# Kernel optimization log

Measured on AMD Instinct MI355X. Metric: run time of the kernel, lower is better.

Reference implementation:

```python
import jax, jax.numpy as jnp
import numpy as np

EMBED_DIM = 1024
NUM_HEADS = 16
HEAD_DIM = EMBED_DIM // NUM_HEADS
WINDOW = 128


def setup_inputs() -> dict:
    key = jax.random.key(0)
    ks = jax.random.split(key, 9)
    B, T, C = 1, 2048, EMBED_DIM
    s = 1.0 / np.sqrt(C)
    inp = {
        "x": jax.random.normal(ks[0], (B, T, C), dtype=jnp.float32),
        "wq": jax.random.normal(ks[1], (C, C), dtype=jnp.float32) * s,
        "bq": jnp.zeros((C,), dtype=jnp.float32),
        "wk": jax.random.normal(ks[2], (C, C), dtype=jnp.float32) * s,
        "bk": jnp.zeros((C,), dtype=jnp.float32),
        "wv": jax.random.normal(ks[3], (C, C), dtype=jnp.float32) * s,
        "bv": jnp.zeros((C,), dtype=jnp.float32),
        "wo": jax.random.normal(ks[4], (C, C), dtype=jnp.float32) * s,
        "bo": jnp.zeros((C,), dtype=jnp.float32),
    }
    return inp


def reference(x, wq, bq, wk, bk, wv, bv, wo, bo):
    B, T, C = x.shape
    H, D, W = NUM_HEADS, HEAD_DIM, WINDOW

    def proj(w, b):
        # torch Linear: y = x @ w.T + b ; -> (B, H, T, D)
        return (x @ w.T + b).reshape(B, T, H, D).transpose(0, 2, 1, 3)

    q = proj(wq, bq)
    k = proj(wk, bk)
    v = proj(wv, bv)

    # window index map: position t attends to keys [t-W+1, t]; zero-padded before 0
    idx = jnp.arange(T)[:, None] + jnp.arange(W)[None, :] - (W - 1)  # (T, W)
    valid = (idx >= 0)
    idxc = jnp.clip(idx, 0, T - 1)

    kw = k[:, :, idxc]                                 # (B, H, T, W, D)
    vw = v[:, :, idxc] * valid[None, None, :, :, None]  # zero padded values

    # zero-key padding gives raw score exactly 0 (inside the softmax)
    scores = jnp.einsum('bhtd,bhtwd->bhtw', q, kw)
    scores = jnp.where(valid[None, None], scores, 0.0) / np.sqrt(D)
    attn = jax.nn.softmax(scores, axis=-1)             # (B, H, T, W)

    ctx = jnp.einsum('bhtw,bhtwd->bhtd', attn, vw)     # (B, H, T, D)
    out = ctx.transpose(0, 2, 1, 3).reshape(B, T, C)
    return out @ wo.T + bo
```

## Files before the change

### kernel.cpp

```cpp
#include <hip/hip_runtime.h>


#define TSEQ 2048
#define CDIM 1024
#define HNUM 16
#define DHEAD 64
#define WWIN 128

typedef __attribute__((ext_vector_type(8))) short bf16x8;
typedef __attribute__((ext_vector_type(4))) float f32x4;

__device__ __forceinline__ unsigned short f2bf(float f) {
  unsigned u = __float_as_uint(f);
  u = (u + 0x7fffu + ((u >> 16) & 1u)) >> 16;
  return (unsigned short)u;
}
__device__ __forceinline__ float bf2f(unsigned short s) {
  return __uint_as_float(((unsigned)s) << 16);
}

__device__ __forceinline__ void gload16(const void* g, void* l) {
  __builtin_amdgcn_global_load_lds(
      (const __attribute__((address_space(1))) unsigned int*)g,
      (__attribute__((address_space(3))) unsigned int*)l, 16, 0, 0);
}

__global__ void split_bf16(const float* s0, const float* s1, const float* s2,
                           const float* s3,
                           unsigned short* h0, unsigned short* h1,
                           unsigned short* h2, unsigned short* h3,
                           unsigned short* l0, unsigned short* l1,
                           unsigned short* l2, unsigned short* l3, int n4) {
  const int z = blockIdx.z;
  const float* __restrict__ src = z == 0 ? s0 : (z == 1 ? s1 : (z == 2 ? s2 : s3));
  unsigned short* __restrict__ h = z == 0 ? h0 : (z == 1 ? h1 : (z == 2 ? h2 : h3));
  unsigned short* __restrict__ l = z == 0 ? l0 : (z == 1 ? l1 : (z == 2 ? l2 : l3));
  const int i = blockIdx.x * 256 + threadIdx.x;
  if (i >= n4) return;
  const float4 v = ((const float4*)src)[i];
  ushort4 hh, ll;
  hh.x = f2bf(v.x); ll.x = f2bf(v.x - bf2f(hh.x));
  hh.y = f2bf(v.y); ll.y = f2bf(v.y - bf2f(hh.y));
  hh.z = f2bf(v.z); ll.z = f2bf(v.z - bf2f(hh.z));
  hh.w = f2bf(v.w); ll.w = f2bf(v.w - bf2f(hh.w));
  ((ushort4*)h)[i] = hh;
  ((ushort4*)l)[i] = ll;
}

__launch_bounds__(256, 2)
__global__ void gemm_mfma_split(const unsigned short* __restrict__ Ah,
                                const unsigned short* __restrict__ Al,
                                const unsigned short* Bh0, const unsigned short* Bh1,
                                const unsigned short* Bh2,
                                const unsigned short* Bl0, const unsigned short* Bl1,
                                const unsigned short* Bl2,
                                const float* bias0, const float* bias1, const float* bias2,
                                float* C0, float* C1, float* C2,
                                int M, int N, int K) {
  const int z = blockIdx.z;
  const unsigned short* __restrict__ Bh = z == 0 ? Bh0 : (z == 1 ? Bh1 : Bh2);
  const unsigned short* __restrict__ Bl = z == 0 ? Bl0 : (z == 1 ? Bl1 : Bl2);
  const float* __restrict__ bias = z == 0 ? bias0 : (z == 1 ? bias1 : bias2);
  float* __restrict__ C = z == 0 ? C0 : (z == 1 ? C1 : C2);

  __shared__ unsigned short lAh[128 * 32], lAl[128 * 32];
  __shared__ unsigned short lBh[128 * 32], lBl[128 * 32];

  const int tid = threadIdx.x;
  const int w = tid >> 6, lane = tid & 63;
  const int wr = w >> 1, wc = w & 1;
  const int bm = blockIdx.y * 128, bn = blockIdx.x * 128;

  int srow[2], scol[2], soff[2];
#pragma unroll
  for (int q = 0; q < 2; ++q) {
    const int s = w * 128 + q * 64 + lane;
    const int r = s >> 2;
    srow[q] = r;
    scol[q] = ((s & 3) ^ ((r >> 1) & 3)) * 8;
    soff[q] = (w * 128 + q * 64) * 8;
  }
  int aoff[4], boff[4];
#pragma unroll
  for (int i = 0; i < 4; ++i) {
    const int ra = wr * 64 + i * 16 + (lane & 15);
    aoff[i] = ra * 32 + (((lane >> 4) ^ ((ra >> 1) & 3)) * 8);
    const int rb = wc * 64 + i * 16 + (lane & 15);
    boff[i] = rb * 32 + (((lane >> 4) ^ ((rb >> 1) & 3)) * 8);
  }

  f32x4 acc[4][4];
#pragma unroll
  for (int i = 0; i < 4; ++i)
#pragma unroll
    for (int j = 0; j < 4; ++j) acc[i][j] = {0.f, 0.f, 0.f, 0.f};

  const unsigned short* gAh = Ah + (size_t)bm * K;
  const unsigned short* gAl = Al + (size_t)bm * K;
  const unsigned short* gBh = Bh + (size_t)bn * K;
  const unsigned short* gBl = Bl + (size_t)bn * K;

  for (int k0 = 0; k0 < K; k0 += 32) {
#pragma unroll
    for (int q = 0; q < 2; ++q) {
      const size_t go = (size_t)srow[q] * K + k0 + scol[q];
      gload16(gAh + go, &lAh[soff[q]]);
      gload16(gAl + go, &lAl[soff[q]]);
      gload16(gBh + go, &lBh[soff[q]]);
      gload16(gBl + go, &lBl[soff[q]]);
    }
    __syncthreads();

    bf16x8 fah[4], fal[4], fbh[4], fbl[4];
#pragma unroll
    for (int i = 0; i < 4; ++i) {
      fah[i] = *(const bf16x8*)&lAh[aoff[i]];
      fal[i] = *(const bf16x8*)&lAl[aoff[i]];
      fbh[i] = *(const bf16x8*)&lBh[boff[i]];
      fbl[i] = *(const bf16x8*)&lBl[boff[i]];
    }
#pragma unroll
    for (int i = 0; i < 4; ++i)
#pragma unroll
      for (int j = 0; j < 4; ++j) {
        acc[i][j] = __builtin_amdgcn_mfma_f32_16x16x32_bf16(fah[i], fbh[j], acc[i][j], 0, 0, 0);
        acc[i][j] = __builtin_amdgcn_mfma_f32_16x16x32_bf16(fah[i], fbl[j], acc[i][j], 0, 0, 0);
        acc[i][j] = __builtin_amdgcn_mfma_f32_16x16x32_bf16(fal[i], fbh[j], acc[i][j], 0, 0, 0);
      }
    __syncthreads();
  }

  const int colb = bn + wc * 64 + (lane & 15);
  const int rowb = bm + wr * 64 + ((lane >> 4) << 2);
#pragma unroll
  for (int j = 0; j < 4; ++j) {
    const int col = colb + j * 16;
    const float bv = bias[col];
#pragma unroll
    for (int i = 0; i < 4; ++i) {
      const int row = rowb + i * 16;
#pragma unroll
      for (int r = 0; r < 4; ++r)
        C[(size_t)(row + r) * N + col] = acc[i][j][r] + bv;
    }
  }
}

__launch_bounds__(256, 2)
__global__ void gemm_bt(const float* __restrict__ A,
                        const float* __restrict__ Bw0, const float* __restrict__ Bw1,
                        const float* __restrict__ Bw2,
                        const float* __restrict__ bias0, const float* __restrict__ bias1,
                        const float* __restrict__ bias2,
                        float* __restrict__ C0, float* __restrict__ C1, float* __restrict__ C2,
                        int M, int N, int K) {
  const int z = blockIdx.z;
  const float* __restrict__ B = (z == 0) ? Bw0 : ((z == 1) ? Bw1 : Bw2);
  const float* __restrict__ bias = (z == 0) ? bias0 : ((z == 1) ? bias1 : bias2);
  float* __restrict__ C = (z == 0) ? C0 : ((z == 1) ? C1 : C2);

  __shared__ float As[16][132];
  __shared__ float Bs[16][132];

  const int tid = threadIdx.x;
  const int tx = tid & 15;
  const int ty = tid >> 4;
  const int bm = blockIdx.y * 128;
  const int bn = blockIdx.x * 128;
  const int lrow = tid >> 2;
  const int lk = (tid & 3) << 2;

  float acc[8][8] = {};

  for (int k0 = 0; k0 < K; k0 += 16) {
#pragma unroll
    for (int r = 0; r < 2; ++r) {
      const int row = (r << 6) + lrow;
      const float4 a4 = *(const float4*)(A + (size_t)(bm + row) * K + k0 + lk);
      As[lk + 0][row] = a4.x; As[lk + 1][row] = a4.y;
      As[lk + 2][row] = a4.z; As[lk + 3][row] = a4.w;
      const float4 b4 = *(const float4*)(B + (size_t)(bn + row) * K + k0 + lk);
      Bs[lk + 0][row] = b4.x; Bs[lk + 1][row] = b4.y;
      Bs[lk + 2][row] = b4.z; Bs[lk + 3][row] = b4.w;
    }
    __syncthreads();
#pragma unroll
    for (int k = 0; k < 16; ++k) {
      float a[8], b[8];
      *(float4*)(a)     = *(const float4*)(&As[k][ty * 8]);
      *(float4*)(a + 4) = *(const float4*)(&As[k][ty * 8 + 4]);
      *(float4*)(b)     = *(const float4*)(&Bs[k][tx * 8]);
      *(float4*)(b + 4) = *(const float4*)(&Bs[k][tx * 8 + 4]);
#pragma unroll
      for (int i = 0; i < 8; ++i)
#pragma unroll
        for (int j = 0; j < 8; ++j)
          acc[i][j] = fmaf(a[i], b[j], acc[i][j]);
    }
    __syncthreads();
  }

#pragma unroll
  for (int i = 0; i < 8; ++i) {
    const int row = bm + ty * 8 + i;
#pragma unroll
    for (int j4 = 0; j4 < 2; ++j4) {
      const int col = bn + tx * 8 + j4 * 4;
      const float4 bb = *(const float4*)(bias + col);
      float4 o;
      o.x = acc[i][j4 * 4 + 0] + bb.x;
      o.y = acc[i][j4 * 4 + 1] + bb.y;
      o.z = acc[i][j4 * 4 + 2] + bb.z;
      o.w = acc[i][j4 * 4 + 3] + bb.w;
      *(float4*)(C + (size_t)row * N + col) = o;
    }
  }
}

__launch_bounds__(256)
__global__ void swa_attn(const float* __restrict__ Q, const float* __restrict__ K,
                         const float* __restrict__ V, float* __restrict__ Of,
                         unsigned short* __restrict__ Oh, unsigned short* __restrict__ Ol,
                         int pack) {
  __shared__ float kb[144 * 64];
  __shared__ float qs[16 * 64];
  __shared__ float ps[4 * 4 * 132];

  const int h = blockIdx.y;
  const int t0 = blockIdx.x * 16;
  const int tid = threadIdx.x;
  const int hoff = h * DHEAD;

  for (int i = tid; i < 144 * 16; i += 256) {
    const int x = i >> 4;
    const int cp = i & 15;
    const int c = cp ^ (x & 15);
    const int key = t0 - (WWIN - 1) + x;
    float4 kv = make_float4(0.f, 0.f, 0.f, 0.f);
    if (key >= 0 && key < TSEQ)
      kv = *(const float4*)(K + (size_t)key * CDIM + hoff + 4 * c);
    *(float4*)&kb[x * 64 + 4 * cp] = kv;
  }
  for (int i = tid; i < 16 * 16; i += 256) {
    const int xq = i >> 4;
    const int c = i & 15;
    *(float4*)&qs[xq * 64 + 4 * c] =
        *(const float4*)(Q + (size_t)(t0 + xq) * CDIM + hoff + 4 * c);
  }
  for (int i = tid; i < 4 * 4 * 132; i += 256) ps[i] = 0.f;
  __syncthreads();

  const int w = tid >> 6;
  const int lane = tid & 63;
  const int q0 = w * 4;

  float inv[4];

#pragma unroll
  for (int q = 0; q < 4; ++q) {
    const int xl = q0 + q + lane;
    const int xm = xl & 15;
    const float* kp0 = kb + xl * 64;
    const float* kp1 = kp0 + 64 * 64;
    const float* qp = qs + (q0 + q) * 64;
    float s0 = 0.f, s1 = 0.f;
#pragma unroll
    for (int dc = 0; dc < 16; ++dc) {
      const float4 qv = *(const float4*)(qp + 4 * dc);
      const int co = 4 * (dc ^ xm);
      const float4 k0 = *(const float4*)(kp0 + co);
      const float4 k1 = *(const float4*)(kp1 + co);
      s0 = fmaf(qv.x, k0.x, fmaf(qv.y, k0.y, fmaf(qv.z, k0.z, fmaf(qv.w, k0.w, s0))));
      s1 = fmaf(qv.x, k1.x, fmaf(qv.y, k1.y, fmaf(qv.z, k1.z, fmaf(qv.w, k1.w, s1))));
    }
    s0 *= 0.125f;
    s1 *= 0.125f;

    float m = fmaxf(s0, s1);
#pragma unroll
    for (int off = 32; off > 0; off >>= 1) m = fmaxf(m, __shfl_xor(m, off));
    const float p0 = __expf(s0 - m);
    const float p1 = __expf(s1 - m);
    float sum = p0 + p1;
#pragma unroll
    for (int off = 32; off > 0; off >>= 1) sum += __shfl_xor(sum, off);
    inv[q] = 1.0f / sum;

    float* psq = ps + (w * 4 + q) * 132;
    psq[q + lane] = p0;
    psq[q + 64 + lane] = p1;
  }

  float accq[4] = {0.f, 0.f, 0.f, 0.f};
  const float* psb = ps + w * 4 * 132;
#pragma unroll 4
  for (int ci = 0; ci < 33; ++ci) {
    const int xr = 4 * ci;
    const float4 pq0 = *(const float4*)(psb + 0 * 132 + xr);
    const float4 pq1 = *(const float4*)(psb + 1 * 132 + xr);
    const float4 pq2 = *(const float4*)(psb + 2 * 132 + xr);
    const float4 pq3 = *(const float4*)(psb + 3 * 132 + xr);
#pragma unroll
    for (int xi = 0; xi < 4; ++xi) {
      const int x = q0 + xr + xi;
      const int key = t0 - (WWIN - 1) + x;
      float vx = 0.f;
      if (key >= 0) {
        const int kc = key < TSEQ ? key : TSEQ - 1;
        vx = V[(size_t)kc * CDIM + hoff + lane];
      }
      const float f0 = (xi == 0) ? pq0.x : (xi == 1) ? pq0.y : (xi == 2) ? pq0.z : pq0.w;
      const float f1 = (xi == 0) ? pq1.x : (xi == 1) ? pq1.y : (xi == 2) ? pq1.z : pq1.w;
      const float f2 = (xi == 0) ? pq2.x : (xi == 1) ? pq2.y : (xi == 2) ? pq2.z : pq2.w;
      const float f3 = (xi == 0) ? pq3.x : (xi == 1) ? pq3.y : (xi == 2) ? pq3.z : pq3.w;
      accq[0] = fmaf(f0, vx, accq[0]);
      accq[1] = fmaf(f1, vx, accq[1]);
      accq[2] = fmaf(f2, vx, accq[2]);
      accq[3] = fmaf(f3, vx, accq[3]);
    }
  }

#pragma unroll
  for (int q = 0; q < 4; ++q) {
    const size_t idx = (size_t)(t0 + q0 + q) * CDIM + hoff + lane;
    const float o = accq[q] * inv[q];
    if (pack) {
      const unsigned short hv = f2bf(o);
      Oh[idx] = hv;
      Ol[idx] = f2bf(o - bf2f(hv));
    } else {
      Of[idx] = o;
    }
  }
}

extern "C" void kernel_launch(void* const* d_in, const int* in_sizes, int n_in,
                              void* d_out, int out_size, void* d_ws, size_t ws_size,
                              hipStream_t stream) {
  const float* x  = (const float*)d_in[0];
  const float* wq = (const float*)d_in[1];
  const float* bq = (const float*)d_in[2];
  const float* wk = (const float*)d_in[3];
  const float* bk = (const float*)d_in[4];
  const float* wv = (const float*)d_in[5];
  const float* bv = (const float*)d_in[6];
  const float* wo = (const float*)d_in[7];
  const float* bo = (const float*)d_in[8];
  float* out = (float*)d_out;

  const size_t MB = 1024 * 1024;
  const size_t NTOK = (size_t)TSEQ * CDIM;

  if (ws_size >= 48 * MB) {
    char* wsb = (char*)d_ws;
    unsigned short* Whq = (unsigned short*)(wsb + 0 * MB);
    unsigned short* Wlq = (unsigned short*)(wsb + 2 * MB);
    unsigned short* Whk = (unsigned short*)(wsb + 4 * MB);
    unsigned short* Wlk = (unsigned short*)(wsb + 6 * MB);
    unsigned short* Whv = (unsigned short*)(wsb + 8 * MB);
    unsigned short* Wlv = (unsigned short*)(wsb + 10 * MB);
    unsigned short* Who = (unsigned short*)(wsb + 12 * MB);
    unsigned short* Wlo = (unsigned short*)(wsb + 14 * MB);
    float* Qw = (float*)(wsb + 16 * MB);
    float* Kw = (float*)(wsb + 24 * MB);
    float* Vw = (float*)(wsb + 32 * MB);
    unsigned short* Ch = (unsigned short*)(wsb + 40 * MB);
    unsigned short* Cl = (unsigned short*)(wsb + 44 * MB);
    unsigned short* Xh = (unsigned short*)d_out;
    unsigned short* Xl = Xh + NTOK;

    {
      dim3 gx((int)(NTOK / 4 / 256), 1, 1);
      split_bf16<<<gx, 256, 0, stream>>>(x, x, x, x, Xh, Xh, Xh, Xh,
                                         Xl, Xl, Xl, Xl, (int)(NTOK / 4));
      const int wn4 = CDIM * CDIM / 4;
      dim3 gw(wn4 / 256, 1, 4);
      split_bf16<<<gw, 256, 0, stream>>>(wq, wk, wv, wo, Whq, Whk, Whv, Who,
                                         Wlq, Wlk, Wlv, Wlo, wn4);
    }

    dim3 gqkv(CDIM / 128, TSEQ / 128, 3);
    gemm_mfma_split<<<gqkv, 256, 0, stream>>>(Xh, Xl, Whq, Whk, Whv, Wlq, Wlk, Wlv,
                                              bq, bk, bv, Qw, Kw, Vw,
                                              TSEQ, CDIM, CDIM);

    dim3 gattn(TSEQ / 16, HNUM);
    swa_attn<<<gattn, 256, 0, stream>>>(Qw, Kw, Vw, (float*)0, Ch, Cl, 1);

    dim3 gout(CDIM / 128, TSEQ / 128, 1);
    gemm_mfma_split<<<gout, 256, 0, stream>>>(Ch, Cl, Who, Who, Who, Wlo, Wlo, Wlo,
                                              bo, bo, bo, out, out, out,
                                              TSEQ, CDIM, CDIM);
  } else {
    float* Qw = (float*)d_ws;
    float* Kw = Qw + NTOK;
    float* Vw = Kw + NTOK;
    float* Cw = Vw + NTOK;

    dim3 gqkv(CDIM / 128, TSEQ / 128, 3);
    gemm_bt<<<gqkv, 256, 0, stream>>>(x, wq, wk, wv, bq, bk, bv, Qw, Kw, Vw,
                                      TSEQ, CDIM, CDIM);

    dim3 gattn(TSEQ / 16, HNUM);
    swa_attn<<<gattn, 256, 0, stream>>>(Qw, Kw, Vw, Cw, (unsigned short*)0,
                                        (unsigned short*)0, 0);

    dim3 gout(CDIM / 128, TSEQ / 128, 1);
    gemm_bt<<<gout, 256, 0, stream>>>(Cw, wo, wo, wo, bo, bo, bo, out, out, out,
                                      TSEQ, CDIM, CDIM);
  }
}
```

Before: 235.2 us.

## Shrink GEMM M-tile to 64 and double attention block query count

The split-bf16 MFMA GEMM now uses 64x128 output tiles instead of 128x128. This doubles the number of blocks so the CUs are better filled, at the cost of less reuse of B tiles. The sliding-window attention kernel now processes 32 queries per block with 512 threads. This amortizes the 127-key halo over twice as many queries, but raises LDS use per block.

```diff
diff --git a/kernel.cpp b/kernel.cpp
--- a/kernel.cpp
+++ b/kernel.cpp
@@ -63,35 +63,42 @@
   const float* __restrict__ bias = z == 0 ? bias0 : (z == 1 ? bias1 : bias2);
   float* __restrict__ C = z == 0 ? C0 : (z == 1 ? C1 : C2);
 
-  __shared__ unsigned short lAh[128 * 32], lAl[128 * 32];
+  __shared__ unsigned short lAh[64 * 32], lAl[64 * 32];
   __shared__ unsigned short lBh[128 * 32], lBl[128 * 32];
 
   const int tid = threadIdx.x;
   const int w = tid >> 6, lane = tid & 63;
   const int wr = w >> 1, wc = w & 1;
-  const int bm = blockIdx.y * 128, bn = blockIdx.x * 128;
-
-  int srow[2], scol[2], soff[2];
+  const int bm = blockIdx.y * 64, bn = blockIdx.x * 128;
+
+  const int sA = tid;
+  const int rA = sA >> 2;
+  const int cA = ((sA & 3) ^ ((rA >> 1) & 3)) * 8;
+  const int oA = (w * 64) * 8;
+  int srowB[2], scolB[2], soffB[2];
 #pragma unroll
   for (int q = 0; q < 2; ++q) {
     const int s = w * 128 + q * 64 + lane;
     const int r = s >> 2;
-    srow[q] = r;
-    scol[q] = ((s & 3) ^ ((r >> 1) & 3)) * 8;
-    soff[q] = (w * 128 + q * 64) * 8;
-  }
-  int aoff[4], boff[4];
-#pragma unroll
-  for (int i = 0; i < 4; ++i) {
-    const int ra = wr * 64 + i * 16 + (lane & 15);
+    srowB[q] = r;
+    scolB[q] = ((s & 3) ^ ((r >> 1) & 3)) * 8;
+    soffB[q] = (w * 128 + q * 64) * 8;
+  }
+  int aoff[2], boff[4];
+#pragma unroll
+  for (int i = 0; i < 2; ++i) {
+    const int ra = wr * 32 + i * 16 + (lane & 15);
     aoff[i] = ra * 32 + (((lane >> 4) ^ ((ra >> 1) & 3)) * 8);
-    const int rb = wc * 64 + i * 16 + (lane & 15);
-    boff[i] = rb * 32 + (((lane >> 4) ^ ((rb >> 1) & 3)) * 8);
-  }
-
-  f32x4 acc[4][4];
-#pragma unroll
-  for (int i = 0; i < 4; ++i)
+  }
+#pragma unroll
+  for (int j = 0; j < 4; ++j) {
+    const int rb = wc * 64 + j * 16 + (lane & 15);
+    boff[j] = rb * 32 + (((lane >> 4) ^ ((rb >> 1) & 3)) * 8);
+  }
+
+  f32x4 acc[2][4];
+#pragma unroll
+  for (int i = 0; i < 2; ++i)
 #pragma unroll
     for (int j = 0; j < 4; ++j) acc[i][j] = {0.f, 0.f, 0.f, 0.f};
 
@@ -101,26 +108,32 @@
   const unsigned short* gBl = Bl + (size_t)bn * K;
 
   for (int k0 = 0; k0 < K; k0 += 32) {
+    {
+      const size_t goA = (size_t)rA * K + k0 + cA;
+      gload16(gAh + goA, &lAh[oA]);
+      gload16(gAl + goA, &lAl[oA]);
+    }
 #pragma unroll
     for (int q = 0; q < 2; ++q) {
-      const size_t go = (size_t)srow[q] * K + k0 + scol[q];
-      gload16(gAh + go, &lAh[soff[q]]);
-      gload16(gAl + go, &lAl[soff[q]]);
-      gload16(gBh + go, &lBh[soff[q]]);
-      gload16(gBl + go, &lBl[soff[q]]);
+      const size_t go = (size_t)srowB[q] * K + k0 + scolB[q];
+      gload16(gBh + go, &lBh[soffB[q]]);
+      gload16(gBl + go, &lBl[soffB[q]]);
     }
     __syncthreads();
 
-    bf16x8 fah[4], fal[4], fbh[4], fbl[4];
-#pragma unroll
-    for (int i = 0; i < 4; ++i) {
+    bf16x8 fah[2], fal[2], fbh[4], fbl[4];
+#pragma unroll
+    for (int i = 0; i < 2; ++i) {
       fah[i] = *(const bf16x8*)&lAh[aoff[i]];
       fal[i] = *(const bf16x8*)&lAl[aoff[i]];
-      fbh[i] = *(const bf16x8*)&lBh[boff[i]];
-      fbl[i] = *(const bf16x8*)&lBl[boff[i]];
-    }
-#pragma unroll
-    for (int i = 0; i < 4; ++i)
+    }
+#pragma unroll
+    for (int j = 0; j < 4; ++j) {
+      fbh[j] = *(const bf16x8*)&lBh[boff[j]];
+      fbl[j] = *(const bf16x8*)&lBl[boff[j]];
+    }
+#pragma unroll
+    for (int i = 0; i < 2; ++i)
 #pragma unroll
       for (int j = 0; j < 4; ++j) {
         acc[i][j] = __builtin_amdgcn_mfma_f32_16x16x32_bf16(fah[i], fbh[j], acc[i][j], 0, 0, 0);
@@ -131,13 +144,13 @@
   }
 
   const int colb = bn + wc * 64 + (lane & 15);
-  const int rowb = bm + wr * 64 + ((lane >> 4) << 2);
+  const int rowb = bm + wr * 32 + ((lane >> 4) << 2);
 #pragma unroll
   for (int j = 0; j < 4; ++j) {
     const int col = colb + j * 16;
     const float bv = bias[col];
 #pragma unroll
-    for (int i = 0; i < 4; ++i) {
+    for (int i = 0; i < 2; ++i) {
       const int row = rowb + i * 16;
 #pragma unroll
       for (int r = 0; r < 4; ++r)
@@ -217,21 +230,21 @@
   }
 }
 
-__launch_bounds__(256)
+__launch_bounds__(512)
 __global__ void swa_attn(const float* __restrict__ Q, const float* __restrict__ K,
                          const float* __restrict__ V, float* __restrict__ Of,
                          unsigned short* __restrict__ Oh, unsigned short* __restrict__ Ol,
                          int pack) {
-  __shared__ float kb[144 * 64];
-  __shared__ float qs[16 * 64];
-  __shared__ float ps[4 * 4 * 132];
+  __shared__ float kb[160 * 64];
+  __shared__ float qs[32 * 64];
+  __shared__ float ps[8 * 4 * 132];
 
   const int h = blockIdx.y;
-  const int t0 = blockIdx.x * 16;
+  const int t0 = blockIdx.x * 32;
   const int tid = threadIdx.x;
   const int hoff = h * DHEAD;
 
-  for (int i = tid; i < 144 * 16; i += 256) {
+  for (int i = tid; i < 160 * 16; i += 512) {
     const int x = i >> 4;
     const int cp = i & 15;
     const int c = cp ^ (x & 15);
@@ -241,13 +254,13 @@
       kv = *(const float4*)(K + (size_t)key * CDIM + hoff + 4 * c);
     *(float4*)&kb[x * 64 + 4 * cp] = kv;
   }
-  for (int i = tid; i < 16 * 16; i += 256) {
+  for (int i = tid; i < 32 * 16; i += 512) {
     const int xq = i >> 4;
     const int c = i & 15;
     *(float4*)&qs[xq * 64 + 4 * c] =
         *(const float4*)(Q + (size_t)(t0 + xq) * CDIM + hoff + 4 * c);
   }
-  for (int i = tid; i < 4 * 4 * 132; i += 256) ps[i] = 0.f;
+  for (int i = tid; i < 8 * 4 * 132; i += 512) ps[i] = 0.f;
   __syncthreads();
 
   const int w = tid >> 6;
@@ -379,15 +392,15 @@
                                          Wlq, Wlk, Wlv, Wlo, wn4);
     }
 
-    dim3 gqkv(CDIM / 128, TSEQ / 128, 3);
+    dim3 gqkv(CDIM / 128, TSEQ / 64, 3);
     gemm_mfma_split<<<gqkv, 256, 0, stream>>>(Xh, Xl, Whq, Whk, Whv, Wlq, Wlk, Wlv,
                                               bq, bk, bv, Qw, Kw, Vw,
                                               TSEQ, CDIM, CDIM);
 
-    dim3 gattn(TSEQ / 16, HNUM);
-    swa_attn<<<gattn, 256, 0, stream>>>(Qw, Kw, Vw, (float*)0, Ch, Cl, 1);
-
-    dim3 gout(CDIM / 128, TSEQ / 128, 1);
+    dim3 gattn(TSEQ / 32, HNUM);
+    swa_attn<<<gattn, 512, 0, stream>>>(Qw, Kw, Vw, (float*)0, Ch, Cl, 1);
+
+    dim3 gout(CDIM / 128, TSEQ / 64, 1);
     gemm_mfma_split<<<gout, 256, 0, stream>>>(Ch, Cl, Who, Who, Who, Wlo, Wlo, Wlo,
                                               bo, bo, bo, out, out, out,
                                               TSEQ, CDIM, CDIM);
@@ -401,8 +414,8 @@
     gemm_bt<<<gqkv, 256, 0, stream>>>(x, wq, wk, wv, bq, bk, bv, Qw, Kw, Vw,
                                       TSEQ, CDIM, CDIM);
 
-    dim3 gattn(TSEQ / 16, HNUM);
-    swa_attn<<<gattn, 256, 0, stream>>>(Qw, Kw, Vw, Cw, (unsigned short*)0,
+    dim3 gattn(TSEQ / 32, HNUM);
+    swa_attn<<<gattn, 512, 0, stream>>>(Qw, Kw, Vw, Cw, (unsigned short*)0,
                                         (unsigned short*)0, 0);
 
     dim3 gout(CDIM / 128, TSEQ / 128, 1);
```

New measurement: 217.2 us. 7.6% less time.
